# Optimization experiments

Hardware: AMD Instinct MI355X
Metric: run time of the kernel (lower is better)

Reference implementation:

```python
import jax, jax.numpy as jnp
import numpy as np

HEADS = 8
DH = 64          # value head dim == kernel head dim (expansion ratio 1.0)
DIM = 256
BOT = 256        # bottleneck_dim
DOUT = 256
HID = 4 * 256    # MLP hidden (expansion_ratio=4)
EPS_LN = 1e-5
EPS_GN = 1e-6


def layer_norm(x, g, b):
    m = x.mean(axis=-1, keepdims=True)
    v = x.var(axis=-1, keepdims=True)
    return (x - m) / jnp.sqrt(v + EPS_LN) * g + b


def rotate_half(x):
    x1, x2 = jnp.split(x, 2, axis=-1)
    return jnp.concatenate([-x2, x1], axis=-1)


def apply_rope(t, cos, sin):
    return t * cos + rotate_half(t) * sin


def mlp(x, W1, b1, W2, b2):
    return jax.nn.gelu(x @ W1 + b1) @ W2 + b2


def pooling_reducer(x, Win, W1, b1, W2, b2):
    # x: (b, n, m, c); mean-pool over axis 2, then MLP
    x = x @ Win
    x = x.mean(axis=2)
    return mlp(x, W1, b1, W2, b2)


def dp_kernel(x, Wqk, cos, sin):
    # x: (b, n, BOT) -> softmax attention kernel (b, h, n, n)
    b, n, _ = x.shape
    qk = (x @ Wqk).reshape(b, n, 2, HEADS, DH).transpose(0, 3, 2, 1, 4)  # b h 2 n d
    qk = apply_rope(qk, cos, sin)
    q, k = qk[:, :, 0], qk[:, :, 1]
    attn = jnp.einsum('bhid,bhjd->bhij', q, k) * (1.0 / DH)  # softmax scale = 1/dim_head
    return jax.nn.softmax(attn, axis=-1)


def group_norm(x):
    # channels-last GroupNorm(heads groups, affine=False), per position
    b, i, l, _ = x.shape
    xg = x.reshape(b, i, l, HEADS, DH)
    m = xg.mean(axis=-1, keepdims=True)
    v = xg.var(axis=-1, keepdims=True)
    return ((xg - m) / jnp.sqrt(v + EPS_GN)).reshape(b, i, l, HEADS * DH)


def setup_inputs() -> dict:
    key = jax.random.key(0)
    ks = jax.random.split(key, 32)
    B, NY, NX = 4, 128, 128
    s = 0.02
    d = {
        'u': jax.random.normal(ks[0], (B, NY, NX, DIM), jnp.float32),
        'rotary_cos_y': jax.random.uniform(ks[1], (NY, DH), jnp.float32),
        'rotary_sin_y': jax.random.uniform(ks[2], (NY, DH), jnp.float32),
        'rotary_cos_x': jax.random.uniform(ks[3], (NX, DH), jnp.float32),
        'rotary_sin_x': jax.random.uniform(ks[4], (NX, DH), jnp.float32),
        'scalar_cond': jax.random.normal(ks[5], (B,), jnp.float32),
        # norms
        'ln1_g': jnp.ones((DIM,), jnp.float32), 'ln1_b': jnp.zeros((DIM,), jnp.float32),
        'ln2_g': jnp.ones((DIM,), jnp.float32), 'ln2_b': jnp.zeros((DIM,), jnp.float32),
        # to_v
        'Wv': jax.random.normal(ks[6], (DIM, HEADS * DH), jnp.float32) * s,
        # to_y PoolingReducer
        'Wy_in': jax.random.normal(ks[7], (DIM, DIM), jnp.float32) * s,
        'Wy1': jax.random.normal(ks[8], (DIM, HID), jnp.float32) * s,
        'by1': jnp.zeros((HID,), jnp.float32),
        'Wy2': jax.random.normal(ks[9], (HID, BOT), jnp.float32) * s,
        'by2': jnp.zeros((BOT,), jnp.float32),
        # to_x PoolingReducer
        'Wx_in': jax.random.normal(ks[10], (DIM, DIM), jnp.float32) * s,
        'Wx1': jax.random.normal(ks[11], (DIM, HID), jnp.float32) * s,
        'bx1': jnp.zeros((HID,), jnp.float32),
        'Wx2': jax.random.normal(ks[12], (HID, BOT), jnp.float32) * s,
        'bx2': jnp.zeros((BOT,), jnp.float32),
        # kernels
        'Wqk_x': jax.random.normal(ks[13], (BOT, 2 * HEADS * DH), jnp.float32) * s,
        'Wqk_y': jax.random.normal(ks[14], (BOT, 2 * HEADS * DH), jnp.float32) * s,
        # merge head
        'Wm': jax.random.normal(ks[15], (HEADS * DH, DOUT), jnp.float32) * s,
        'bm': jnp.zeros((DOUT,), jnp.float32),
        # ffn
        'Wf1': jax.random.normal(ks[16], (DOUT, 4 * DOUT), jnp.float32) * s,
        'bf1': jnp.zeros((4 * DOUT,), jnp.float32),
        'Wf2': jax.random.normal(ks[17], (4 * DOUT, DOUT), jnp.float32) * s,
        'bf2': jnp.zeros((DOUT,), jnp.float32),
    }
    return d


def reference(u, rotary_cos_y, rotary_sin_y, rotary_cos_x, rotary_sin_x, scalar_cond,
              ln1_g, ln1_b, ln2_g, ln2_b, Wv,
              Wy_in, Wy1, by1, Wy2, by2,
              Wx_in, Wx1, bx1, Wx2, bx2,
              Wqk_x, Wqk_y, Wm, bm, Wf1, bf1, Wf2, bf2):
    b, ny, nx, _ = u.shape
    u_skip = u
    un = layer_norm(u, ln1_g, ln1_b)
    # to_x: transpose grid then pool over (now) second spatial axis -> (b, nx, BOT)
    u_x = pooling_reducer(un.transpose(0, 2, 1, 3), Wx_in, Wx1, bx1, Wx2, bx2)
    # to_y: pool over nx -> (b, ny, BOT)
    u_y = pooling_reducer(un, Wy_in, Wy1, by1, Wy2, by2)
    k_x = dp_kernel(u_x, Wqk_x, rotary_cos_x, rotary_sin_x)  # (b,h,nx,nx)
    k_y = dp_kernel(u_y, Wqk_y, rotary_cos_y, rotary_sin_y)  # (b,h,ny,ny)
    # values: b i l (h c) -> b h i l c
    v = (un @ Wv).reshape(b, ny, nx, HEADS, DH).transpose(0, 3, 1, 2, 4)
    u_phi = jnp.einsum('bhij,bhjmc->bhimc', k_y, v)
    u_phi = jnp.einsum('bhlm,bhimc->bhilc', k_x, u_phi)
    u_phi = u_phi.transpose(0, 2, 3, 1, 4).reshape(b, ny, nx, HEADS * DH)
    u2 = group_norm(u_phi) @ Wm + bm + u_skip  # dropout is identity in eval
    out = mlp(layer_norm(u2, ln2_g, ln2_b), Wf1, bf1, Wf2, bf2) + u2
    return out
```

## Files before the change

### kernel.cpp

```cpp
#include <hip/hip_runtime.h>
#include <hip/hip_bf16.h>
#include <math.h>

#define NB 4
#define NY 128
#define NX 128
#define DIM 256
#define NH 8
#define DH_ 64
#define HDIM 512
#define HID 1024
#define NPOS (NB*NY*NX)

typedef __hip_bfloat16 bf16_t;
typedef __attribute__((ext_vector_type(8))) short short8;
typedef __attribute__((ext_vector_type(4))) float f32x4;

__device__ __forceinline__ float b2f(bf16_t x){ return __bfloat162float(x); }
__device__ __forceinline__ bf16_t f2b(float x){ return __float2bfloat16(x); }
__device__ __forceinline__ short f2s(float x){ bf16_t h = __float2bfloat16(x); return *reinterpret_cast<short*>(&h); }
__device__ __forceinline__ float s2f(short x){ bf16_t h = *reinterpret_cast<bf16_t*>(&x); return __bfloat162float(h); }


__device__ __forceinline__ float gelu_tanh(float x){
  float z = 1.5957691216057308f*(x + 0.044715f*x*x*x);
  return x / (1.0f + __expf(-z));
}

__global__ void __launch_bounds__(256) k_pack(const float* __restrict__ W,
    short* __restrict__ out, int K, int N){
  int tid = blockIdx.x*256 + threadIdx.x;
  int lane = tid & 63;
  int rem = tid >> 6;
  int ntiles = N >> 4;
  int nt = rem % ntiles, kb = rem / ntiles;
  int n = nt*16 + (lane & 15);
  int k0 = kb*32 + (lane>>4)*8;
  short8 v;
  #pragma unroll
  for (int j=0;j<8;j++) v[j] = f2s(W[(size_t)(k0+j)*N + n]);
  *(short8*)&out[(size_t)tid*8] = v;
}

__global__ void __launch_bounds__(256) k_ln1(const float* __restrict__ u,
    const float* __restrict__ g, const float* __restrict__ b,
    bf16_t* __restrict__ un){
  int wave = threadIdx.x >> 6, lane = threadIdx.x & 63;
  size_t row = (size_t)blockIdx.x*4 + wave;
  const float* x = u + row*DIM;
  float v[4]; float s=0.f, ss=0.f;
  #pragma unroll
  for (int j=0;j<4;j++){ float t = x[lane + j*64]; v[j]=t; s+=t; ss+=t*t; }
  #pragma unroll
  for (int off=32;off>0;off>>=1){ s += __shfl_down(s,off,64); ss += __shfl_down(ss,off,64); }
  s = __shfl(s,0,64); ss = __shfl(ss,0,64);
  float m = s*(1.0f/DIM);
  float var = ss*(1.0f/DIM) - m*m;
  float r = rsqrtf(var + 1e-5f);
  bf16_t* o = un + row*DIM;
  #pragma unroll
  for (int j=0;j<4;j++){
    int f = lane + j*64;
    o[f] = f2b((v[j]-m)*r*g[f] + b[f]);
  }
}

__global__ void __launch_bounds__(256) k_pool_y(const bf16_t* __restrict__ un, float* __restrict__ pooly){
  int by = blockIdx.x;
  int d = threadIdx.x;
  size_t base = (size_t)by*NX*DIM + d;
  float s = 0.f;
  for (int x=0;x<NX;x++) s += b2f(un[base + (size_t)x*DIM]);
  pooly[(size_t)by*DIM + d] = s*(1.0f/NX);
}
__global__ void __launch_bounds__(256) k_pool_x(const bf16_t* __restrict__ un, float* __restrict__ poolx){
  int bb = blockIdx.x / NX, x = blockIdx.x % NX;
  int d = threadIdx.x;
  size_t base = ((size_t)bb*NY*NX + x)*DIM + d;
  float s = 0.f;
  for (int y=0;y<NY;y++) s += b2f(un[base + (size_t)y*NX*DIM]);
  poolx[(size_t)blockIdx.x*DIM + d] = s*(1.0f/NY);
}

#define GS_STRIDE 72
__global__ void __launch_bounds__(256) k_gemm2(const float* __restrict__ A0,
    const float* __restrict__ A1,
    const short* __restrict__ W0, const short* __restrict__ W1,
    const float* __restrict__ b0, const float* __restrict__ b1,
    float* __restrict__ C0, float* __restrict__ C1, int N, int K, int dogelu){
  const float* A  = blockIdx.z ? A1 : A0;
  const short* WP = blockIdx.z ? W1 : W0;
  const float* bias = blockIdx.z ? b1 : b0;
  float* C = blockIdx.z ? C1 : C0;
  __shared__ __align__(16) short As[64*GS_STRIDE];
  int tid = threadIdx.x;
  int lane = tid & 63, w = tid >> 6;
  int am = lane & 15, aq = lane >> 4;
  int m0 = blockIdx.x*64;
  int nt0 = blockIdx.y*16;
  int ntiles = N >> 4;
  f32x4 o[4][4];
  #pragma unroll
  for (int mt=0;mt<4;mt++)
    #pragma unroll
    for (int nt=0;nt<4;nt++) o[mt][nt] = (f32x4){0.f,0.f,0.f,0.f};

  for (int kc=0; kc<K; kc+=64){
    #pragma unroll
    for (int it=0; it<4; it++){
      int q = tid + it*256;
      int r = q >> 4, c4 = q & 15;
      float4 v = *(const float4*)&A[(size_t)(m0+r)*K + kc + c4*4];
      ushort4 p;
      p.x = (ushort)f2s(v.x); p.y = (ushort)f2s(v.y);
      p.z = (ushort)f2s(v.z); p.w = (ushort)f2s(v.w);
      *(ushort4*)&As[r*GS_STRIDE + c4*4] = p;
    }
    __syncthreads();
    #pragma unroll
    for (int kb=0; kb<2; kb++){
      short8 a[4], bfr[4];
      #pragma unroll
      for (int mt=0;mt<4;mt++)
        a[mt] = *(const short8*)&As[(mt*16+am)*GS_STRIDE + kb*32 + aq*8];
      int kbg = (kc>>5) + kb;
      #pragma unroll
      for (int nt=0;nt<4;nt++){
        int ntg = nt0 + w*4 + nt;
        bfr[nt] = *(const short8*)&WP[(size_t)((kbg*ntiles + ntg)*64 + lane)*8];
      }
      #pragma unroll
      for (int mt=0;mt<4;mt++)
        #pragma unroll
        for (int nt=0;nt<4;nt++)
          o[mt][nt] = __builtin_amdgcn_mfma_f32_16x16x32_bf16(a[mt], bfr[nt], o[mt][nt], 0,0,0);
    }
    __syncthreads();
  }

  #pragma unroll
  for (int nt=0;nt<4;nt++){
    int col = (nt0 + w*4 + nt)*16 + am;
    float bv = bias ? bias[col] : 0.f;
    #pragma unroll
    for (int mt=0;mt<4;mt++){
      #pragma unroll
      for (int reg=0;reg<4;reg++){
        int row = m0 + mt*16 + aq*4 + reg;
        float val = o[mt][nt][reg] + bv;
        if (dogelu) val = gelu_tanh(val);
        C[(size_t)row*N + col] = val;
      }
    }
  }
}

__global__ void __launch_bounds__(256) k_rope(const float* __restrict__ qk,
    const float* __restrict__ cs, const float* __restrict__ sn,
    float* __restrict__ q, float* __restrict__ k){
  int idx = blockIdx.x*256 + threadIdx.x;
  int c = idx & 63;
  int h = (idx>>6) & 7;
  int p = (idx>>9) & 1;
  int n = (idx>>10) & 127;
  int bb = idx>>17;
  float t = qk[idx];
  float t2 = qk[(c<32) ? idx+32 : idx-32];
  if (c<32) t2 = -t2;
  float val = t*cs[n*64+c] + t2*sn[n*64+c];
  float* dst = p ? k : q;
  dst[(((size_t)bb*NH + h)*128 + n)*64 + c] = val;
}

__global__ void __launch_bounds__(128) k_attn(const float* __restrict__ q,
    const float* __restrict__ k, bf16_t* __restrict__ attn){
  int i = blockIdx.x & 127;
  int bh = blockIdx.x >> 7;
  __shared__ float qs[64];
  __shared__ float red[4];
  int tid = threadIdx.x;
  int wv = tid >> 6, lane = tid & 63;
  const float* qrow = q + ((size_t)bh*128 + i)*64;
  if (tid < 64) qs[tid] = qrow[tid];
  __syncthreads();
  const float* krow = k + ((size_t)bh*128 + tid)*64;
  float dot = 0.f;
  for (int c=0;c<64;c++) dot += qs[c]*krow[c];
  dot *= (1.0f/64.0f);
  float mx = dot;
  #pragma unroll
  for (int off=32;off>0;off>>=1) mx = fmaxf(mx, __shfl_xor(mx, off, 64));
  if (lane == 0) red[wv] = mx;
  __syncthreads();
  mx = fmaxf(red[0], red[1]);
  float e = __expf(dot - mx);
  float s = e;
  #pragma unroll
  for (int off=32;off>0;off>>=1) s += __shfl_xor(s, off, 64);
  if (lane == 0) red[2+wv] = s;
  __syncthreads();
  s = red[2] + red[3];
  attn[(size_t)blockIdx.x*128 + tid] = f2b(e/s);
}

#define AST 136
#define UST 72
#define VST 136
__global__ void __launch_bounds__(512) k_phi1m(const bf16_t* __restrict__ un,
    const short* __restrict__ WvP, const bf16_t* __restrict__ attn,
    bf16_t* __restrict__ phi){
  int m  = blockIdx.x & (NX-1);
  int bh = blockIdx.x >> 7;
  int b  = bh >> 3, h = bh & 7;
  __shared__ __align__(16) short At[128*AST];
  __shared__ __align__(16) short unc[128*UST];
  __shared__ __align__(16) short Vt[64*VST];
  int tid = threadIdx.x;
  int lane = tid & 63, w = tid >> 6;
  int am = lane & 15, aq = lane >> 4;

  {
    const ushort* ag = (const ushort*)attn + (size_t)bh*16384;
    #pragma unroll
    for (int it=0; it<8; it++){
      int q = tid + it*512;
      int i = q >> 5, j4 = q & 31;
      *(ushort4*)&At[i*AST + j4*4] = *(const ushort4*)(ag + i*128 + j4*4);
    }
  }

  f32x4 v[4];
  #pragma unroll
  for (int nt=0;nt<4;nt++) v[nt] = (f32x4){0.f,0.f,0.f,0.f};
  const ushort* ug = (const ushort*)un;
  for (int kc=0; kc<4; kc++){
    #pragma unroll
    for (int it=0; it<4; it++){
      int q = tid + it*512;
      int y = q >> 4, c4 = q & 15;
      *(ushort4*)&unc[y*UST + c4*4] =
          *(const ushort4*)(ug + (((size_t)b*NY + y)*NX + m)*DIM + kc*64 + c4*4);
    }
    __syncthreads();
    #pragma unroll
    for (int kb=0; kb<2; kb++){
      short8 a2 = *(const short8*)&unc[(w*16 + am)*UST + kb*32 + aq*8];
      int kbg = kc*2 + kb;
      short8 bb[4];
      #pragma unroll
      for (int nt=0;nt<4;nt++)
        bb[nt] = *(const short8*)&WvP[(size_t)((kbg*32 + (h*4+nt))*64 + lane)*8];
      #pragma unroll
      for (int nt=0;nt<4;nt++)
        v[nt] = __builtin_amdgcn_mfma_f32_16x16x32_bf16(a2, bb[nt], v[nt], 0,0,0);
    }
    __syncthreads();
  }
  #pragma unroll
  for (int nt=0;nt<4;nt++){
    int c = nt*16 + am;
    int y0 = w*16 + aq*4;
    ushort4 pk;
    pk.x = (ushort)f2s(v[nt][0]);
    pk.y = (ushort)f2s(v[nt][1]);
    pk.z = (ushort)f2s(v[nt][2]);
    pk.w = (ushort)f2s(v[nt][3]);
    *(ushort4*)&Vt[c*VST + y0] = pk;
  }
  __syncthreads();

  f32x4 o[4];
  #pragma unroll
  for (int nt=0;nt<4;nt++) o[nt] = (f32x4){0.f,0.f,0.f,0.f};
  #pragma unroll
  for (int kb=0; kb<4; kb++){
    short8 a2 = *(const short8*)&At[(w*16 + am)*AST + kb*32 + aq*8];
    short8 bb[4];
    #pragma unroll
    for (int nt=0;nt<4;nt++)
      bb[nt] = *(const short8*)&Vt[(nt*16 + am)*VST + kb*32 + aq*8];
    #pragma unroll
    for (int nt=0;nt<4;nt++)
      o[nt] = __builtin_amdgcn_mfma_f32_16x16x32_bf16(a2, bb[nt], o[nt], 0,0,0);
  }
  ushort* pg = (ushort*)phi + (size_t)bh*NY*NX*DH_ + (size_t)m*DH_;
  #pragma unroll
  for (int nt=0;nt<4;nt++)
    #pragma unroll
    for (int reg=0;reg<4;reg++){
      int i = w*16 + aq*4 + reg;
      int c = nt*16 + am;
      pg[(size_t)i*(NX*DH_) + c] = (ushort)f2s(o[nt][reg]);
    }
}

__global__ void __launch_bounds__(512) k_phi2m(const bf16_t* __restrict__ attn,
    bf16_t* __restrict__ phi){
  int i  = blockIdx.x & (NY-1);
  int bh = blockIdx.x >> 7;
  __shared__ __align__(16) short Ax[128*AST];
  __shared__ __align__(16) short Pt[64*VST];
  int tid = threadIdx.x;
  int lane = tid & 63, w = tid >> 6;
  int am = lane & 15, aq = lane >> 4;

  {
    const ushort* ag = (const ushort*)attn + (size_t)bh*16384;
    #pragma unroll
    for (int it=0; it<8; it++){
      int q = tid + it*512;
      int r = q >> 5, j4 = q & 31;
      *(ushort4*)&Ax[r*AST + j4*4] = *(const ushort4*)(ag + r*128 + j4*4);
    }
  }
  ushort* pg = (ushort*)phi + (size_t)(bh*NY + i)*(NX*DH_);
  #pragma unroll
  for (int it=0; it<4; it++){
    int q = tid + it*512;
    int mm = q >> 4, c4 = q & 15;
    ushort4 v4 = *(const ushort4*)(pg + mm*DH_ + c4*4);
    Pt[(c4*4+0)*VST + mm] = v4.x;
    Pt[(c4*4+1)*VST + mm] = v4.y;
    Pt[(c4*4+2)*VST + mm] = v4.z;
    Pt[(c4*4+3)*VST + mm] = v4.w;
  }
  __syncthreads();

  f32x4 o[4];
  #pragma unroll
  for (int nt=0;nt<4;nt++) o[nt] = (f32x4){0.f,0.f,0.f,0.f};
  #pragma unroll
  for (int kb=0; kb<4; kb++){
    short8 a2 = *(const short8*)&Ax[(w*16 + am)*AST + kb*32 + aq*8];
    short8 bb[4];
    #pragma unroll
    for (int nt=0;nt<4;nt++)
      bb[nt] = *(const short8*)&Pt[(nt*16 + am)*VST + kb*32 + aq*8];
    #pragma unroll
    for (int nt=0;nt<4;nt++)
      o[nt] = __builtin_amdgcn_mfma_f32_16x16x32_bf16(a2, bb[nt], o[nt], 0,0,0);
  }
  #pragma unroll
  for (int nt=0;nt<4;nt++)
    #pragma unroll
    for (int reg=0;reg<4;reg++){
      int l = w*16 + aq*4 + reg;
      int c = nt*16 + am;
      pg[(size_t)l*DH_ + c] = (ushort)f2s(o[nt][reg]);
    }
}

#define GN_ST 520
#define ML_ST 264
__global__ void __launch_bounds__(1024, 8) k_tail(const bf16_t* __restrict__ phi,
    const short* __restrict__ WmP, const float* __restrict__ bm,
    const float* __restrict__ u,
    const float* __restrict__ g2, const float* __restrict__ b2,
    const short* __restrict__ Wf1P, const float* __restrict__ bf1,
    const short* __restrict__ Wf2P, const float* __restrict__ bf2,
    float* __restrict__ out){
  __shared__ __align__(16) short SMEM[64*ML_ST*2];
  __shared__ float mean_s[512], rstd_s[512];
  __shared__ float prow[64][8], prow2[64][8];
  __shared__ float mrow[64], rrow[64];
  short* Xg = SMEM;
  short* Xm = SMEM;
  short* H  = SMEM + 64*ML_ST;
  int tid = threadIdx.x;
  int lane = tid & 63, w = tid >> 6;
  int wh = w >> 3, wl = w & 7;
  int am = lane & 15, aq = lane >> 4;
  size_t p0 = (size_t)blockIdx.x*64;
  int b  = (int)(p0 >> 14);
  int y  = (int)((p0 >> 7) & 127);
  int x0 = (int)(p0 & 127);

  #pragma unroll
  for (int it=0; it<8; it++){
    int q = tid + it*1024;
    int r = q >> 7, f4 = q & 127;
    int h = f4 >> 4, c4 = f4 & 15;
    const ushort* src = (const ushort*)phi +
        ((((size_t)b*NH + h)*NY + y)*NX + (x0 + r))*DH_ + c4*4;
    *(ushort4*)&Xg[r*GN_ST + f4*4] = *(const ushort4*)src;
  }
  __syncthreads();
  if (tid < 512){
    int g = tid;
    int r = g >> 3, h = g & 7;
    const short* base = &Xg[r*GN_ST + h*64];
    float s=0.f, ss=0.f;
    #pragma unroll
    for (int i=0;i<16;i++){
      ushort4 v4 = *(const ushort4*)&base[i*4];
      float a = s2f((short)v4.x), bq = s2f((short)v4.y), cq = s2f((short)v4.z), d = s2f((short)v4.w);
      s += a+bq+cq+d; ss += a*a+bq*bq+cq*cq+d*d;
    }
    float mm = s*(1.0f/64.0f);
    float vv = ss*(1.0f/64.0f) - mm*mm;
    mean_s[g] = mm;
    rstd_s[g] = rsqrtf(vv + 1e-6f);
  }
  __syncthreads();
  #pragma unroll
  for (int it=0; it<8; it++){
    int q = tid + it*1024;
    int r = q >> 7, f4 = q & 127;
    int h = f4 >> 4;
    float mm = mean_s[r*8 + h], rs = rstd_s[r*8 + h];
    short* ptr = &Xg[r*GN_ST + f4*4];
    ushort4 v4 = *(ushort4*)ptr;
    v4.x = (ushort)f2s((s2f((short)v4.x)-mm)*rs);
    v4.y = (ushort)f2s((s2f((short)v4.y)-mm)*rs);
    v4.z = (ushort)f2s((s2f((short)v4.z)-mm)*rs);
    v4.w = (ushort)f2s((s2f((short)v4.w)-mm)*rs);
    *(ushort4*)ptr = v4;
  }
  __syncthreads();

  f32x4 u2r[2][2];
  #pragma unroll
  for (int mt=0;mt<2;mt++)
    #pragma unroll
    for (int nt=0;nt<2;nt++) u2r[mt][nt] = (f32x4){0.f,0.f,0.f,0.f};
  for (int kb=0; kb<16; kb++){
    short8 a[2], bfr[2];
    #pragma unroll
    for (int mt=0;mt<2;mt++)
      a[mt] = *(const short8*)&Xg[(wh*32 + mt*16 + am)*GN_ST + kb*32 + aq*8];
    #pragma unroll
    for (int nt=0;nt<2;nt++)
      bfr[nt] = *(const short8*)&WmP[(size_t)((kb*16 + (wl*2+nt))*64 + lane)*8];
    #pragma unroll
    for (int mt=0;mt<2;mt++)
      #pragma unroll
      for (int nt=0;nt<2;nt++)
        u2r[mt][nt] = __builtin_amdgcn_mfma_f32_16x16x32_bf16(a[mt], bfr[nt], u2r[mt][nt], 0,0,0);
  }
  #pragma unroll
  for (int nt=0;nt<2;nt++){
    int col = wl*32 + nt*16 + am;
    float bmv = bm[col];
    #pragma unroll
    for (int mt=0;mt<2;mt++){
      #pragma unroll
      for (int reg=0;reg<4;reg++){
        size_t p = p0 + wh*32 + mt*16 + aq*4 + reg;
        u2r[mt][nt][reg] += bmv + u[p*DIM + col];
      }
    }
  }

  #pragma unroll
  for (int mt=0;mt<2;mt++){
    #pragma unroll
    for (int reg=0;reg<4;reg++){
      float s  = u2r[mt][0][reg]+u2r[mt][1][reg];
      float ss = u2r[mt][0][reg]*u2r[mt][0][reg]+u2r[mt][1][reg]*u2r[mt][1][reg];
      #pragma unroll
      for (int msk=1; msk<16; msk<<=1){
        s  += __shfl_xor(s,  msk, 64);
        ss += __shfl_xor(ss, msk, 64);
      }
      if (am == 0){
        int r = wh*32 + mt*16 + aq*4 + reg;
        prow[r][wl] = s;
        prow2[r][wl] = ss;
      }
    }
  }
  __syncthreads();
  if (tid < 64){
    float s = 0.f, ss = 0.f;
    #pragma unroll
    for (int j=0;j<8;j++){ s += prow[tid][j]; ss += prow2[tid][j]; }
    float m = s*(1.0f/DIM);
    mrow[tid] = m;
    rrow[tid] = rsqrtf(ss*(1.0f/DIM) - m*m + 1e-5f);
  }
  __syncthreads();
  #pragma unroll
  for (int nt=0;nt<2;nt++){
    int col = wl*32 + nt*16 + am;
    float gg = g2[col], bb2 = b2[col];
    #pragma unroll
    for (int mt=0;mt<2;mt++){
      #pragma unroll
      for (int reg=0;reg<4;reg++){
        int r = wh*32 + mt*16 + aq*4 + reg;
        Xm[r*ML_ST + col] = f2s((u2r[mt][nt][reg]-mrow[r])*rrow[r]*gg + bb2);
      }
    }
  }
  __syncthreads();

  f32x4 o2[2][2];
  #pragma unroll
  for (int mt=0;mt<2;mt++)
    #pragma unroll
    for (int nt=0;nt<2;nt++) o2[mt][nt] = u2r[mt][nt];

  for (int nc=0; nc<4; nc++){
    f32x4 hacc[2][2];
    #pragma unroll
    for (int mt=0;mt<2;mt++)
      #pragma unroll
      for (int nt=0;nt<2;nt++) hacc[mt][nt] = (f32x4){0.f,0.f,0.f,0.f};
    for (int kb=0; kb<8; kb++){
      short8 a[2], bfr[2];
      #pragma unroll
      for (int mt=0;mt<2;mt++)
        a[mt] = *(const short8*)&Xm[(wh*32 + mt*16 + am)*ML_ST + kb*32 + aq*8];
      #pragma unroll
      for (int nt=0;nt<2;nt++){
        int ntg = nc*16 + wl*2 + nt;
        bfr[nt] = *(const short8*)&Wf1P[(size_t)((kb*64 + ntg)*64 + lane)*8];
      }
      #pragma unroll
      for (int mt=0;mt<2;mt++)
        #pragma unroll
        for (int nt=0;nt<2;nt++)
          hacc[mt][nt] = __builtin_amdgcn_mfma_f32_16x16x32_bf16(a[mt], bfr[nt], hacc[mt][nt], 0,0,0);
    }
    #pragma unroll
    for (int nt=0;nt<2;nt++){
      int col_l = wl*32 + nt*16 + am;
      float bv = bf1[nc*256 + col_l];
      #pragma unroll
      for (int mt=0;mt<2;mt++){
        #pragma unroll
        for (int reg=0;reg<4;reg++){
          int row = wh*32 + mt*16 + aq*4 + reg;
          H[row*ML_ST + col_l] = f2s(gelu_tanh(hacc[mt][nt][reg] + bv));
        }
      }
    }
    __syncthreads();
    for (int kb=0; kb<8; kb++){
      short8 a[2], bfr[2];
      #pragma unroll
      for (int mt=0;mt<2;mt++)
        a[mt] = *(const short8*)&H[(wh*32 + mt*16 + am)*ML_ST + kb*32 + aq*8];
      int kbg = nc*8 + kb;
      #pragma unroll
      for (int nt=0;nt<2;nt++)
        bfr[nt] = *(const short8*)&Wf2P[(size_t)((kbg*16 + (wl*2+nt))*64 + lane)*8];
      #pragma unroll
      for (int mt=0;mt<2;mt++)
        #pragma unroll
        for (int nt=0;nt<2;nt++)
          o2[mt][nt] = __builtin_amdgcn_mfma_f32_16x16x32_bf16(a[mt], bfr[nt], o2[mt][nt], 0,0,0);
    }
    __syncthreads();
  }

  #pragma unroll
  for (int nt=0;nt<2;nt++){
    int col = wl*32 + nt*16 + am;
    float bv = bf2[col];
    #pragma unroll
    for (int mt=0;mt<2;mt++){
      #pragma unroll
      for (int reg=0;reg<4;reg++){
        size_t p = p0 + wh*32 + mt*16 + aq*4 + reg;
        out[p*DIM + col] = o2[mt][nt][reg] + bv;
      }
    }
  }
}

extern "C" void kernel_launch(void* const* d_in, const int* in_sizes, int n_in,
                              void* d_out, int out_size, void* d_ws, size_t ws_size,
                              hipStream_t stream){
  const float* u    = (const float*)d_in[0];
  const float* rcy  = (const float*)d_in[1];
  const float* rsy  = (const float*)d_in[2];
  const float* rcx  = (const float*)d_in[3];
  const float* rsx  = (const float*)d_in[4];
  const float* ln1g = (const float*)d_in[6];
  const float* ln1b = (const float*)d_in[7];
  const float* ln2g = (const float*)d_in[8];
  const float* ln2b = (const float*)d_in[9];
  const float* Wv   = (const float*)d_in[10];
  const float* Wyin = (const float*)d_in[11];
  const float* Wy1  = (const float*)d_in[12];
  const float* by1  = (const float*)d_in[13];
  const float* Wy2  = (const float*)d_in[14];
  const float* by2  = (const float*)d_in[15];
  const float* Wxin = (const float*)d_in[16];
  const float* Wx1  = (const float*)d_in[17];
  const float* bx1  = (const float*)d_in[18];
  const float* Wx2  = (const float*)d_in[19];
  const float* bx2  = (const float*)d_in[20];
  const float* Wqkx = (const float*)d_in[21];
  const float* Wqky = (const float*)d_in[22];
  const float* Wm   = (const float*)d_in[23];
  const float* bm   = (const float*)d_in[24];
  const float* Wf1  = (const float*)d_in[25];
  const float* bf1  = (const float*)d_in[26];
  const float* Wf2  = (const float*)d_in[27];
  const float* bf2  = (const float*)d_in[28];

  char* w = (char*)d_ws;
  auto alloc = [&](size_t n) -> void* {
    void* p = (void*)w;
    w += (n + 255) & ~(size_t)255;
    return p;
  };
  bf16_t* UN   = (bf16_t*)alloc((size_t)NPOS*DIM*2);
  bf16_t* PHI  = (bf16_t*)alloc((size_t)NB*NH*NY*NX*DH_*2);
  float* POOLY = (float*)alloc((size_t)NB*NY*DIM*4);
  float* POOLX = (float*)alloc((size_t)NB*NX*DIM*4);
  float* TY    = (float*)alloc((size_t)512*256*4);
  float* TX    = (float*)alloc((size_t)512*256*4);
  float* HY    = (float*)alloc((size_t)512*1024*4);
  float* HX    = (float*)alloc((size_t)512*1024*4);
  float* UY    = (float*)alloc((size_t)512*256*4);
  float* UX    = (float*)alloc((size_t)512*256*4);
  float* QKY   = (float*)alloc((size_t)512*1024*4);
  float* QKX   = (float*)alloc((size_t)512*1024*4);
  float* QRY   = (float*)alloc((size_t)NB*NH*128*64*4);
  float* KRY   = (float*)alloc((size_t)NB*NH*128*64*4);
  float* QRX   = (float*)alloc((size_t)NB*NH*128*64*4);
  float* KRX   = (float*)alloc((size_t)NB*NH*128*64*4);
  bf16_t* ATTNY = (bf16_t*)alloc((size_t)NB*NH*128*128*2);
  bf16_t* ATTNX = (bf16_t*)alloc((size_t)NB*NH*128*128*2);
  short* WF1P  = (short*)alloc((size_t)256*1024*2);
  short* WF2P  = (short*)alloc((size_t)1024*256*2);
  short* WMP   = (short*)alloc((size_t)512*256*2);
  short* WVP   = (short*)alloc((size_t)256*512*2);
  short* WYINP = (short*)alloc((size_t)256*256*2);
  short* WY1P  = (short*)alloc((size_t)256*1024*2);
  short* WY2P  = (short*)alloc((size_t)1024*256*2);
  short* WQKYP = (short*)alloc((size_t)256*1024*2);
  short* WXINP = (short*)alloc((size_t)256*256*2);
  short* WX1P  = (short*)alloc((size_t)256*1024*2);
  short* WX2P  = (short*)alloc((size_t)1024*256*2);
  short* WQKXP = (short*)alloc((size_t)256*1024*2);
  float* U2 = (float*)d_out;
  (void)in_sizes; (void)n_in; (void)out_size; (void)ws_size;

  k_pack<<<(256*1024/8)/256, 256, 0, stream>>>(Wf1, WF1P, 256, 1024);
  k_pack<<<(1024*256/8)/256, 256, 0, stream>>>(Wf2, WF2P, 1024, 256);
  k_pack<<<(512*256/8)/256, 256, 0, stream>>>(Wm, WMP, 512, 256);
  k_pack<<<(256*512/8)/256, 256, 0, stream>>>(Wv, WVP, 256, 512);
  k_pack<<<(256*256/8)/256, 256, 0, stream>>>(Wyin, WYINP, 256, 256);
  k_pack<<<(256*1024/8)/256, 256, 0, stream>>>(Wy1, WY1P, 256, 1024);
  k_pack<<<(1024*256/8)/256, 256, 0, stream>>>(Wy2, WY2P, 1024, 256);
  k_pack<<<(256*1024/8)/256, 256, 0, stream>>>(Wqky, WQKYP, 256, 1024);
  k_pack<<<(256*256/8)/256, 256, 0, stream>>>(Wxin, WXINP, 256, 256);
  k_pack<<<(256*1024/8)/256, 256, 0, stream>>>(Wx1, WX1P, 256, 1024);
  k_pack<<<(1024*256/8)/256, 256, 0, stream>>>(Wx2, WX2P, 1024, 256);
  k_pack<<<(256*1024/8)/256, 256, 0, stream>>>(Wqkx, WQKXP, 256, 1024);

  k_ln1<<<NPOS/4, 256, 0, stream>>>(u, ln1g, ln1b, UN);
  k_pool_y<<<NB*NY, 256, 0, stream>>>(UN, POOLY);
  k_pool_x<<<NB*NX, 256, 0, stream>>>(UN, POOLX);

  k_gemm2<<<dim3(8,1,2), 256, 0, stream>>>(POOLY, POOLX, WYINP, WXINP,
      (const float*)nullptr, (const float*)nullptr, TY, TX, 256, 256, 0);
  k_gemm2<<<dim3(8,4,2), 256, 0, stream>>>(TY, TX, WY1P, WX1P, by1, bx1, HY, HX, 1024, 256, 1);
  k_gemm2<<<dim3(8,1,2), 256, 0, stream>>>(HY, HX, WY2P, WX2P, by2, bx2, UY, UX, 256, 1024, 0);
  k_gemm2<<<dim3(8,4,2), 256, 0, stream>>>(UY, UX, WQKYP, WQKXP,
      (const float*)nullptr, (const float*)nullptr, QKY, QKX, 1024, 256, 0);

  k_rope<<<(NB*128*1024)/256, 256, 0, stream>>>(QKY, rcy, rsy, QRY, KRY);
  k_rope<<<(NB*128*1024)/256, 256, 0, stream>>>(QKX, rcx, rsx, QRX, KRX);
  k_attn<<<NB*NH*128, 128, 0, stream>>>(QRY, KRY, ATTNY);
  k_attn<<<NB*NH*128, 128, 0, stream>>>(QRX, KRX, ATTNX);
  k_phi1m<<<NB*NH*NX, 512, 0, stream>>>(UN, WVP, ATTNY, PHI);
  k_phi2m<<<NB*NH*NY, 512, 0, stream>>>(ATTNX, PHI);
  k_tail<<<NPOS/64, 1024, 0, stream>>>(PHI, WMP, bm, u, ln2g, ln2b,
      WF1P, bf1, WF2P, bf2, U2);
}
```

Baseline: 664.1 us.

## Fuse GroupNorm into phi2 epilogue and shrink tail kernel to 512 threads

The per-head GroupNorm moves out of the tail kernel and into the k_phi2m epilogue. Each output row's 64 channels sit in one wave's MFMA accumulators, so mean and variance come from 16-lane shuffles and the normalized value is written straight to PHI. This removes two shared-memory passes and two barriers from k_tail. k_tail also drops from 16 to 8 waves, with each wave covering 64 output columns instead of 32, which doubles B-fragment loads per wave and raises accumulator register use.

```diff
diff --git a/kernel.cpp b/kernel.cpp
--- a/kernel.cpp
+++ b/kernel.cpp
@@ -341,6 +341,23 @@
       o[nt] = __builtin_amdgcn_mfma_f32_16x16x32_bf16(a2, bb[nt], o[nt], 0,0,0);
   }
   #pragma unroll
+  for (int reg=0;reg<4;reg++){
+    float s  = o[0][reg]+o[1][reg]+o[2][reg]+o[3][reg];
+    float ss = o[0][reg]*o[0][reg]+o[1][reg]*o[1][reg]
+             + o[2][reg]*o[2][reg]+o[3][reg]*o[3][reg];
+    #pragma unroll
+    for (int msk=1; msk<16; msk<<=1){
+      s  += __shfl_xor(s,  msk, 64);
+      ss += __shfl_xor(ss, msk, 64);
+    }
+    float mm = s*(1.0f/64.0f);
+    float vv = ss*(1.0f/64.0f) - mm*mm;
+    float rs = rsqrtf(vv + 1e-6f);
+    #pragma unroll
+    for (int nt=0;nt<4;nt++)
+      o[nt][reg] = (o[nt][reg]-mm)*rs;
+  }
+  #pragma unroll
   for (int nt=0;nt<4;nt++)
     #pragma unroll
     for (int reg=0;reg<4;reg++){
@@ -352,7 +369,7 @@
 
 #define GN_ST 520
 #define ML_ST 264
-__global__ void __launch_bounds__(1024, 8) k_tail(const bf16_t* __restrict__ phi,
+__global__ void __launch_bounds__(512, 4) k_tail(const bf16_t* __restrict__ phi,
     const short* __restrict__ WmP, const float* __restrict__ bm,
     const float* __restrict__ u,
     const float* __restrict__ g2, const float* __restrict__ b2,
@@ -360,15 +377,14 @@
     const short* __restrict__ Wf2P, const float* __restrict__ bf2,
     float* __restrict__ out){
   __shared__ __align__(16) short SMEM[64*ML_ST*2];
-  __shared__ float mean_s[512], rstd_s[512];
-  __shared__ float prow[64][8], prow2[64][8];
+  __shared__ float prow[64][4], prow2[64][4];
   __shared__ float mrow[64], rrow[64];
   short* Xg = SMEM;
   short* Xm = SMEM;
   short* H  = SMEM + 64*ML_ST;
   int tid = threadIdx.x;
   int lane = tid & 63, w = tid >> 6;
-  int wh = w >> 3, wl = w & 7;
+  int wh = w >> 2, wl = w & 3;
   int am = lane & 15, aq = lane >> 4;
   size_t p0 = (size_t)blockIdx.x*64;
   int b  = (int)(p0 >> 14);
@@ -376,70 +392,38 @@
   int x0 = (int)(p0 & 127);
 
   #pragma unroll
-  for (int it=0; it<8; it++){
-    int q = tid + it*1024;
+  for (int it=0; it<16; it++){
+    int q = tid + it*512;
     int r = q >> 7, f4 = q & 127;
     int h = f4 >> 4, c4 = f4 & 15;
-    const ushort* src = (const ushort*)phi +
-        ((((size_t)b*NH + h)*NY + y)*NX + (x0 + r))*DH_ + c4*4;
-    *(ushort4*)&Xg[r*GN_ST + f4*4] = *(const ushort4*)src;
-  }
-  __syncthreads();
-  if (tid < 512){
-    int g = tid;
-    int r = g >> 3, h = g & 7;
-    const short* base = &Xg[r*GN_ST + h*64];
-    float s=0.f, ss=0.f;
-    #pragma unroll
-    for (int i=0;i<16;i++){
-      ushort4 v4 = *(const ushort4*)&base[i*4];
-      float a = s2f((short)v4.x), bq = s2f((short)v4.y), cq = s2f((short)v4.z), d = s2f((short)v4.w);
-      s += a+bq+cq+d; ss += a*a+bq*bq+cq*cq+d*d;
-    }
-    float mm = s*(1.0f/64.0f);
-    float vv = ss*(1.0f/64.0f) - mm*mm;
-    mean_s[g] = mm;
-    rstd_s[g] = rsqrtf(vv + 1e-6f);
-  }
-  __syncthreads();
-  #pragma unroll
-  for (int it=0; it<8; it++){
-    int q = tid + it*1024;
-    int r = q >> 7, f4 = q & 127;
-    int h = f4 >> 4;
-    float mm = mean_s[r*8 + h], rs = rstd_s[r*8 + h];
-    short* ptr = &Xg[r*GN_ST + f4*4];
-    ushort4 v4 = *(ushort4*)ptr;
-    v4.x = (ushort)f2s((s2f((short)v4.x)-mm)*rs);
-    v4.y = (ushort)f2s((s2f((short)v4.y)-mm)*rs);
-    v4.z = (ushort)f2s((s2f((short)v4.z)-mm)*rs);
-    v4.w = (ushort)f2s((s2f((short)v4.w)-mm)*rs);
-    *(ushort4*)ptr = v4;
-  }
-  __syncthreads();
-
-  f32x4 u2r[2][2];
+    size_t gi = (((size_t)b*NH + h)*NY + y)*NX + (x0 + r);
+    *(ushort4*)&Xg[r*GN_ST + f4*4] =
+        *(const ushort4*)((const ushort*)phi + gi*DH_ + c4*4);
+  }
+  __syncthreads();
+
+  f32x4 u2r[2][4];
   #pragma unroll
   for (int mt=0;mt<2;mt++)
     #pragma unroll
-    for (int nt=0;nt<2;nt++) u2r[mt][nt] = (f32x4){0.f,0.f,0.f,0.f};
+    for (int nt=0;nt<4;nt++) u2r[mt][nt] = (f32x4){0.f,0.f,0.f,0.f};
   for (int kb=0; kb<16; kb++){
-    short8 a[2], bfr[2];
+    short8 a[2], bfr[4];
     #pragma unroll
     for (int mt=0;mt<2;mt++)
       a[mt] = *(const short8*)&Xg[(wh*32 + mt*16 + am)*GN_ST + kb*32 + aq*8];
     #pragma unroll
-    for (int nt=0;nt<2;nt++)
-      bfr[nt] = *(const short8*)&WmP[(size_t)((kb*16 + (wl*2+nt))*64 + lane)*8];
+    for (int nt=0;nt<4;nt++)
+      bfr[nt] = *(const short8*)&WmP[(size_t)((kb*16 + (wl*4+nt))*64 + lane)*8];
     #pragma unroll
     for (int mt=0;mt<2;mt++)
       #pragma unroll
-      for (int nt=0;nt<2;nt++)
+      for (int nt=0;nt<4;nt++)
         u2r[mt][nt] = __builtin_amdgcn_mfma_f32_16x16x32_bf16(a[mt], bfr[nt], u2r[mt][nt], 0,0,0);
   }
   #pragma unroll
-  for (int nt=0;nt<2;nt++){
-    int col = wl*32 + nt*16 + am;
+  for (int nt=0;nt<4;nt++){
+    int col = wl*64 + nt*16 + am;
     float bmv = bm[col];
     #pragma unroll
     for (int mt=0;mt<2;mt++){
@@ -455,8 +439,9 @@
   for (int mt=0;mt<2;mt++){
     #pragma unroll
     for (int reg=0;reg<4;reg++){
-      float s  = u2r[mt][0][reg]+u2r[mt][1][reg];
-      float ss = u2r[mt][0][reg]*u2r[mt][0][reg]+u2r[mt][1][reg]*u2r[mt][1][reg];
+      float s  = u2r[mt][0][reg]+u2r[mt][1][reg]+u2r[mt][2][reg]+u2r[mt][3][reg];
+      float ss = u2r[mt][0][reg]*u2r[mt][0][reg]+u2r[mt][1][reg]*u2r[mt][1][reg]
+               + u2r[mt][2][reg]*u2r[mt][2][reg]+u2r[mt][3][reg]*u2r[mt][3][reg];
       #pragma unroll
       for (int msk=1; msk<16; msk<<=1){
         s  += __shfl_xor(s,  msk, 64);
@@ -471,17 +456,16 @@
   }
   __syncthreads();
   if (tid < 64){
-    float s = 0.f, ss = 0.f;
-    #pragma unroll
-    for (int j=0;j<8;j++){ s += prow[tid][j]; ss += prow2[tid][j]; }
+    float s  = prow[tid][0]+prow[tid][1]+prow[tid][2]+prow[tid][3];
+    float ss = prow2[tid][0]+prow2[tid][1]+prow2[tid][2]+prow2[tid][3];
     float m = s*(1.0f/DIM);
     mrow[tid] = m;
     rrow[tid] = rsqrtf(ss*(1.0f/DIM) - m*m + 1e-5f);
   }
   __syncthreads();
   #pragma unroll
-  for (int nt=0;nt<2;nt++){
-    int col = wl*32 + nt*16 + am;
+  for (int nt=0;nt<4;nt++){
+    int col = wl*64 + nt*16 + am;
     float gg = g2[col], bb2 = b2[col];
     #pragma unroll
     for (int mt=0;mt<2;mt++){
@@ -494,37 +478,37 @@
   }
   __syncthreads();
 
-  f32x4 o2[2][2];
+  f32x4 o2[2][4];
   #pragma unroll
   for (int mt=0;mt<2;mt++)
     #pragma unroll
-    for (int nt=0;nt<2;nt++) o2[mt][nt] = u2r[mt][nt];
+    for (int nt=0;nt<4;nt++) o2[mt][nt] = u2r[mt][nt];
 
   for (int nc=0; nc<4; nc++){
-    f32x4 hacc[2][2];
+    f32x4 hacc[2][4];
     #pragma unroll
     for (int mt=0;mt<2;mt++)
       #pragma unroll
-      for (int nt=0;nt<2;nt++) hacc[mt][nt] = (f32x4){0.f,0.f,0.f,0.f};
+      for (int nt=0;nt<4;nt++) hacc[mt][nt] = (f32x4){0.f,0.f,0.f,0.f};
     for (int kb=0; kb<8; kb++){
-      short8 a[2], bfr[2];
+      short8 a[2], bfr[4];
       #pragma unroll
       for (int mt=0;mt<2;mt++)
         a[mt] = *(const short8*)&Xm[(wh*32 + mt*16 + am)*ML_ST + kb*32 + aq*8];
       #pragma unroll
-      for (int nt=0;nt<2;nt++){
-        int ntg = nc*16 + wl*2 + nt;
+      for (int nt=0;nt<4;nt++){
+        int ntg = nc*16 + wl*4 + nt;
         bfr[nt] = *(const short8*)&Wf1P[(size_t)((kb*64 + ntg)*64 + lane)*8];
       }
       #pragma unroll
       for (int mt=0;mt<2;mt++)
         #pragma unroll
-        for (int nt=0;nt<2;nt++)
+        for (int nt=0;nt<4;nt++)
           hacc[mt][nt] = __builtin_amdgcn_mfma_f32_16x16x32_bf16(a[mt], bfr[nt], hacc[mt][nt], 0,0,0);
     }
     #pragma unroll
-    for (int nt=0;nt<2;nt++){
-      int col_l = wl*32 + nt*16 + am;
+    for (int nt=0;nt<4;nt++){
+      int col_l = wl*64 + nt*16 + am;
       float bv = bf1[nc*256 + col_l];
       #pragma unroll
       for (int mt=0;mt<2;mt++){
@@ -537,26 +521,26 @@
     }
     __syncthreads();
     for (int kb=0; kb<8; kb++){
-      short8 a[2], bfr[2];
+      short8 a[2], bfr[4];
       #pragma unroll
       for (int mt=0;mt<2;mt++)
         a[mt] = *(const short8*)&H[(wh*32 + mt*16 + am)*ML_ST + kb*32 + aq*8];
       int kbg = nc*8 + kb;
       #pragma unroll
-      for (int nt=0;nt<2;nt++)
-        bfr[nt] = *(const short8*)&Wf2P[(size_t)((kbg*16 + (wl*2+nt))*64 + lane)*8];
+      for (int nt=0;nt<4;nt++)
+        bfr[nt] = *(const short8*)&Wf2P[(size_t)((kbg*16 + (wl*4+nt))*64 + lane)*8];
       #pragma unroll
       for (int mt=0;mt<2;mt++)
         #pragma unroll
-        for (int nt=0;nt<2;nt++)
+        for (int nt=0;nt<4;nt++)
           o2[mt][nt] = __builtin_amdgcn_mfma_f32_16x16x32_bf16(a[mt], bfr[nt], o2[mt][nt], 0,0,0);
     }
     __syncthreads();
   }
 
   #pragma unroll
-  for (int nt=0;nt<2;nt++){
-    int col = wl*32 + nt*16 + am;
+  for (int nt=0;nt<4;nt++){
+    int col = wl*64 + nt*16 + am;
     float bv = bf2[col];
     #pragma unroll
     for (int mt=0;mt<2;mt++){
@@ -670,6 +654,6 @@
   k_attn<<<NB*NH*128, 128, 0, stream>>>(QRX, KRX, ATTNX);
   k_phi1m<<<NB*NH*NX, 512, 0, stream>>>(UN, WVP, ATTNY, PHI);
   k_phi2m<<<NB*NH*NY, 512, 0, stream>>>(ATTNX, PHI);
-  k_tail<<<NPOS/64, 1024, 0, stream>>>(PHI, WMP, bm, u, ln2g, ln2b,
+  k_tail<<<NPOS/64, 512, 0, stream>>>(PHI, WMP, bm, u, ln2g, ln2b,
       WF1P, bf1, WF2P, bf2, U2);
 }
```

Measured after the change: 620.4 us. 1.07x faster.
